# Performance work log

Hardware: AMD Instinct MI355X
Metric: run time of the kernel (lower is better)

## Reference

```python
import jax, jax.numpy as jnp
import numpy as np

N = 8192       # tokens (batch*seq)
D = 4096       # input_size / d_model
H = 256        # gate hidden_size
E = 64         # num_experts
K = 2          # top_k


def setup_inputs() -> dict:
    key = jax.random.key(0)
    k0, k1, k2, k3 = jax.random.split(key, 4)
    x = jax.random.normal(k0, (N, D), dtype=jnp.float32)
    # nn.Linear default init: U(-1/sqrt(fan_in), 1/sqrt(fan_in))
    w1 = jax.random.uniform(k1, (H, D), jnp.float32, -1.0, 1.0) / np.sqrt(D)
    b1 = jax.random.uniform(k2, (H,), jnp.float32, -1.0, 1.0) / np.sqrt(D)
    w2 = jax.random.uniform(k3, (E, H), jnp.float32, -1.0, 1.0) / np.sqrt(H)
    return {"x": x, "w1": w1, "b1": b1, "w2": w2}


def reference(x, w1, b1, w2):
    # MLP gate: Linear -> GELU (exact erf, torch default) -> Dropout(eval: identity) -> Linear(no bias)
    h = jax.nn.gelu(jnp.einsum('nd,hd->nh', x, w1) + b1, approximate=False)  # [N, H]
    logits = jnp.einsum('nh,eh->ne', h, w2)                                  # [N, E]
    probs = jax.nn.softmax(logits, axis=-1)                                  # [N, E]
    # deterministic top-k path (sample_topk=0 / eval mode)
    top_k_gates, top_k_indices = jax.lax.top_k(probs, K)                     # [N, K] each
    return top_k_indices, top_k_gates, probs
```

## Files before the change

kernel.cpp:

```cpp
#include <hip/hip_runtime.h>
#include <hip/hip_bf16.h>
#include <math.h>

#define NTOK 8192
#define DIN  4096
#define HG   256
#define NE   64
#define SPLITK 4
#define KSTEPS 32
#define TR   16

typedef __attribute__((ext_vector_type(8))) short short8;
typedef __attribute__((ext_vector_type(4))) float f32x4;

__device__ __forceinline__ unsigned short f2bf_rne(float f) {
    union { float f; unsigned int u; } v; v.f = f;
    unsigned int r = v.u + 0x7fffu + ((v.u >> 16) & 1u);
    return (unsigned short)(r >> 16);
}
__device__ __forceinline__ float bf2f(unsigned short b) {
    union { unsigned int u; float f; } v; v.u = ((unsigned int)b) << 16;
    return v.f;
}

typedef const __attribute__((address_space(1))) unsigned int* gptr_t;
typedef __attribute__((address_space(3))) unsigned int* lptr_t;
__device__ __forceinline__ void gload_lds16(const void* g, void* l) {
    __builtin_amdgcn_global_load_lds((gptr_t)g, (lptr_t)l, 16, 0, 0);
}

#define WAIT_VMCNT4 { asm volatile("s_waitcnt vmcnt(4)" ::: "memory"); \
                      __builtin_amdgcn_sched_barrier(0); }
#define WAIT_VMCNT0 { asm volatile("s_waitcnt vmcnt(0)" ::: "memory"); \
                      __builtin_amdgcn_sched_barrier(0); }
#define WAIT_LGKM0  { asm volatile("s_waitcnt lgkmcnt(0)" ::: "memory"); \
                      __builtin_amdgcn_sched_barrier(0); }

__global__ __launch_bounds__(512) void convert_w1_kernel(
    const float* __restrict__ w1, unsigned short* __restrict__ w1t)
{
    const int id    = blockIdx.x * 512 + threadIdx.x;
    const int lane  = id & 63;
    const int cg    = id >> 6;
    const int kstep = cg >> 5;
    const int c     = cg & 31;
    const int hl    = c >> 4;
    const int unit  = c & 15;
    const int n     = unit * 16 + (lane & 15);
    const int k     = kstep * 32 + ((lane >> 4) & 3) * 8;

    const float* src = w1 + (size_t)n * DIN + k;
    short8 v;
#pragma unroll
    for (int j = 0; j < 8; ++j) {
        float f = src[j];
        unsigned short hi = f2bf_rne(f);
        v[j] = (hl == 0) ? (short)hi : (short)f2bf_rne(f - bf2f(hi));
    }
    *(short8*)(w1t + (size_t)cg * 512 + lane * 8) = v;
}

__global__ __launch_bounds__(512, 2) void gemm1_mfma_kernel(
    const float* __restrict__ x, const unsigned short* __restrict__ w1t,
    float* __restrict__ P)
{
    __shared__ unsigned short As[2][2][8][512];
    __shared__ unsigned short Bs[3][2][16][512];

    const int bid  = blockIdx.x;
    const int s    = (bid & 7) >> 1;
    const int mblk = ((bid >> 3) << 1) | (bid & 1);
    const int t    = threadIdx.x;
    const int lane = t & 63;
    const int w    = t >> 6;
    const int wm   = w >> 2;
    const int wn   = w & 3;

    const int m_base = mblk * 128;
    const int kstep0 = s * KSTEPS;

    const int a_unit = t >> 6;
    const int a_q    = t & 63;
    const int a_row  = a_unit * 16 + (a_q & 15);
    const int a_koff = (a_q >> 4) * 8;
    const float* asrc = x + (size_t)(m_base + a_row) * DIN
                          + (size_t)kstep0 * 32 + a_koff;
    const int a_ldso = a_q * 8;

    f32x4 acc[4][4];
#pragma unroll
    for (int i = 0; i < 4; ++i)
#pragma unroll
        for (int j = 0; j < 4; ++j) acc[i][j] = (f32x4)0.f;

#define CVT8_STORE(BUF, F0, F1)                                               \
    {   short8 vh_, vl_;                                                      \
        float ff_[8] = { (F0).x, (F0).y, (F0).z, (F0).w,                      \
                         (F1).x, (F1).y, (F1).z, (F1).w };                    \
        _Pragma("unroll")                                                     \
        for (int j_ = 0; j_ < 8; ++j_) {                                      \
            unsigned short h_ = f2bf_rne(ff_[j_]);                            \
            vh_[j_] = (short)h_;                                              \
            vl_[j_] = (short)f2bf_rne(ff_[j_] - bf2f(h_));                    \
        }                                                                     \
        *(short8*)&As[BUF][0][a_unit][a_ldso] = vh_;                          \
        *(short8*)&As[BUF][1][a_unit][a_ldso] = vl_;                          \
    }

#define ISSUE_B(KS, BUF)                                                      \
    _Pragma("unroll")                                                         \
    for (int i_ = 0; i_ < 4; ++i_) {                                          \
        const int c_ = w * 4 + i_;                                            \
        gload_lds16(w1t + ((size_t)(KS) * 32 + c_) * 512 + lane * 8,          \
                    &Bs[BUF][c_ >> 4][c_ & 15][0]);                           \
    }

    {
        float4 a0 = *(const float4*)(asrc);
        float4 a1 = *(const float4*)(asrc + 4);
        ISSUE_B(kstep0, 0)
        CVT8_STORE(0, a0, a1)
        ISSUE_B(kstep0 + 1, 1)
        WAIT_VMCNT4
        WAIT_LGKM0
        __builtin_amdgcn_s_barrier();
    }

    int bcur = 0, bnx1 = 1, bnx2 = 2;
    int acur = 0;

#pragma unroll 1
    for (int tt = 0; tt < KSTEPS; ++tt) {
        const bool has1 = (tt + 1 < KSTEPS);
        const bool has2 = (tt + 2 < KSTEPS);

        float4 nx0, nx1;
        if (has1) {
            const float* ap = asrc + (size_t)(tt + 1) * 32;
            nx0 = *(const float4*)(ap);
            nx1 = *(const float4*)(ap + 4);
        }
        if (has2) { ISSUE_B(kstep0 + tt + 2, bnx2) }

        short8 ahf[4], alf[4], bhf[4], blf[4];
#pragma unroll
        for (int mr = 0; mr < 4; ++mr) {
            ahf[mr] = *(const short8*)&As[acur][0][wm * 4 + mr][lane * 8];
            alf[mr] = *(const short8*)&As[acur][1][wm * 4 + mr][lane * 8];
        }
#pragma unroll
        for (int nr = 0; nr < 4; ++nr) {
            bhf[nr] = *(const short8*)&Bs[bcur][0][wn * 4 + nr][lane * 8];
            blf[nr] = *(const short8*)&Bs[bcur][1][wn * 4 + nr][lane * 8];
        }

        __builtin_amdgcn_s_setprio(1);
#pragma unroll
        for (int mr = 0; mr < 4; ++mr)
#pragma unroll
            for (int nr = 0; nr < 4; ++nr)
                acc[mr][nr] = __builtin_amdgcn_mfma_f32_16x16x32_bf16(
                    ahf[mr], bhf[nr], acc[mr][nr], 0, 0, 0);
#pragma unroll
        for (int mr = 0; mr < 4; ++mr)
#pragma unroll
            for (int nr = 0; nr < 4; ++nr)
                acc[mr][nr] = __builtin_amdgcn_mfma_f32_16x16x32_bf16(
                    ahf[mr], blf[nr], acc[mr][nr], 0, 0, 0);
#pragma unroll
        for (int mr = 0; mr < 4; ++mr)
#pragma unroll
            for (int nr = 0; nr < 4; ++nr)
                acc[mr][nr] = __builtin_amdgcn_mfma_f32_16x16x32_bf16(
                    alf[mr], bhf[nr], acc[mr][nr], 0, 0, 0);
        __builtin_amdgcn_s_setprio(0);

        if (has1) {
            CVT8_STORE(acur ^ 1, nx0, nx1)
            if (has2) { WAIT_VMCNT4 }
            else      { WAIT_VMCNT0 }
            WAIT_LGKM0
            __builtin_amdgcn_s_barrier();
        }

        const int z = bcur; bcur = bnx1; bnx1 = bnx2; bnx2 = z;
        acur ^= 1;
    }
#undef ISSUE_B
#undef CVT8_STORE

    float* pb = P + (size_t)s * ((size_t)NTOK * HG);
#pragma unroll
    for (int mr = 0; mr < 4; ++mr)
#pragma unroll
        for (int nr = 0; nr < 4; ++nr) {
            const int n = wn * 64 + nr * 16 + (lane & 15);
#pragma unroll
            for (int r = 0; r < 4; ++r) {
                const int m = m_base + wm * 64 + mr * 16 + ((lane >> 4) & 3) * 4 + r;
                pb[(size_t)m * HG + n] = acc[mr][nr][r];
            }
        }
}

__global__ __launch_bounds__(512, 4) void reduce_gate_kernel(
    const float* __restrict__ P, const float* __restrict__ b1,
    const float* __restrict__ w2, float* __restrict__ out)
{
    __shared__ float h_lds[TR][260];
    __shared__ float lg[NE][33];

    const int t    = threadIdx.x;
    const int lane = t & 63;
    const int w    = t >> 6;
    const int r0   = blockIdx.x * TR;
    const size_t SS = (size_t)NTOK * HG;

    {
        const int row = t >> 5;
        const int sg  = t & 31;
        const size_t base = (size_t)(r0 + row) * HG + sg * 8;

        float q[8];
#pragma unroll
        for (int half = 0; half < 2; ++half) {
            float4 v0 = *(const float4*)(P + base + half * 4);
            float4 v1 = *(const float4*)(P + base + SS + half * 4);
            float4 v2 = *(const float4*)(P + base + 2 * SS + half * 4);
            float4 v3 = *(const float4*)(P + base + 3 * SS + half * 4);
            float4 bb = *(const float4*)(b1 + sg * 8 + half * 4);
            q[half * 4 + 0] = v0.x + v1.x + v2.x + v3.x + bb.x;
            q[half * 4 + 1] = v0.y + v1.y + v2.y + v3.y + bb.y;
            q[half * 4 + 2] = v0.z + v1.z + v2.z + v3.z + bb.z;
            q[half * 4 + 3] = v0.w + v1.w + v2.w + v3.w + bb.w;
        }
#pragma unroll
        for (int c = 0; c < 8; ++c)
            q[c] = 0.5f * q[c] * (1.0f + erff(q[c] * 0.70710678118654752440f));

        *(float4*)&h_lds[row][sg * 8]     = make_float4(q[0], q[1], q[2], q[3]);
        *(float4*)&h_lds[row][sg * 8 + 4] = make_float4(q[4], q[5], q[6], q[7]);
    }
    __syncthreads();

    const int e0   = w * 8;
    const int rowp = lane & 15;
    const int kq   = lane >> 4;

    float acc[8];
#pragma unroll
    for (int i = 0; i < 8; ++i) acc[i] = 0.f;

    const float* w2b = w2 + (size_t)e0 * HG + kq * 64;
#pragma unroll 1
    for (int kc = 0; kc < 64; kc += 8) {
        float a[8];
        *(float4*)&a[0] = *(const float4*)&h_lds[rowp][kq * 64 + kc];
        *(float4*)&a[4] = *(const float4*)&h_lds[rowp][kq * 64 + kc + 4];
#pragma unroll
        for (int n = 0; n < 8; ++n) {
            const float* wr = w2b + (size_t)n * HG + kc;
            float4 w0 = *(const float4*)(wr);
            float4 w1v = *(const float4*)(wr + 4);
            acc[n] = fmaf(w0.x, a[0], acc[n]);
            acc[n] = fmaf(w0.y, a[1], acc[n]);
            acc[n] = fmaf(w0.z, a[2], acc[n]);
            acc[n] = fmaf(w0.w, a[3], acc[n]);
            acc[n] = fmaf(w1v.x, a[4], acc[n]);
            acc[n] = fmaf(w1v.y, a[5], acc[n]);
            acc[n] = fmaf(w1v.z, a[6], acc[n]);
            acc[n] = fmaf(w1v.w, a[7], acc[n]);
        }
    }
#pragma unroll
    for (int n = 0; n < 8; ++n) {
        acc[n] += __shfl_xor(acc[n], 16);
        acc[n] += __shfl_xor(acc[n], 32);
    }
    if (lane < 16) {
#pragma unroll
        for (int n = 0; n < 8; ++n) lg[e0 + n][rowp] = acc[n];
    }
    __syncthreads();

    if (t < TR) {
        float l[NE];
#pragma unroll
        for (int e = 0; e < NE; ++e) l[e] = lg[e][t];

        float mx = l[0];
#pragma unroll
        for (int e = 1; e < NE; ++e) mx = fmaxf(mx, l[e]);

        float ssum = 0.f;
#pragma unroll
        for (int e = 0; e < NE; ++e) { float p = expf(l[e] - mx); l[e] = p; ssum += p; }
        const float inv = 1.0f / ssum;
#pragma unroll
        for (int e = 0; e < NE; ++e) l[e] *= inv;

        float v1 = -1.0f, v2 = -2.0f;
        int   i1 = 0,     i2 = 0;
#pragma unroll
        for (int e = 0; e < NE; ++e) {
            const float p  = l[e];
            const bool  g1 = p > v1;
            const bool  g2 = p > v2;
            const float nv2 = g1 ? v1 : (g2 ? p : v2);
            const int   ni2 = g1 ? i1 : (g2 ? e : i2);
            v1 = g1 ? p : v1;
            i1 = g1 ? e : i1;
            v2 = nv2;
            i2 = ni2;
        }

        const int row = r0 + t;
        float* out_idx  = out;
        float* out_gate = out + 2 * NTOK;
        float* out_prob = out + 4 * NTOK;
        out_idx[2 * row + 0]  = (float)i1;
        out_idx[2 * row + 1]  = (float)i2;
        out_gate[2 * row + 0] = v1;
        out_gate[2 * row + 1] = v2;

        float* pr = out_prob + (size_t)row * NE;
#pragma unroll
        for (int e = 0; e < NE; e += 4)
            *(float4*)(pr + e) = make_float4(l[e], l[e + 1], l[e + 2], l[e + 3]);
    }
}

extern "C" void kernel_launch(void* const* d_in, const int* in_sizes, int n_in,
                              void* d_out, int out_size, void* d_ws, size_t ws_size,
                              hipStream_t stream) {
    const float* x  = (const float*)d_in[0];
    const float* w1 = (const float*)d_in[1];
    const float* b1 = (const float*)d_in[2];
    const float* w2 = (const float*)d_in[3];
    float* out = (float*)d_out;

    unsigned short* w1t = (unsigned short*)d_ws;
    float* P = (float*)((char*)d_ws + (4u << 20));

    convert_w1_kernel<<<512, 512, 0, stream>>>(w1, w1t);
    gemm1_mfma_kernel<<<256, 512, 0, stream>>>(x, w1t, P);
    reduce_gate_kernel<<<512, 512, 0, stream>>>(P, b1, w2, out);
}
```

Baseline: 104.3 us.

## Shrink GEMM1 tiles to 64 rows and drop multi-buffered async B pipeline

```diff
diff --git a/kernel.cpp b/kernel.cpp
--- a/kernel.cpp
+++ b/kernel.cpp
@@ -29,8 +29,6 @@
     __builtin_amdgcn_global_load_lds((gptr_t)g, (lptr_t)l, 16, 0, 0);
 }
 
-#define WAIT_VMCNT4 { asm volatile("s_waitcnt vmcnt(4)" ::: "memory"); \
-                      __builtin_amdgcn_sched_barrier(0); }
 #define WAIT_VMCNT0 { asm volatile("s_waitcnt vmcnt(0)" ::: "memory"); \
                       __builtin_amdgcn_sched_barrier(0); }
 #define WAIT_LGKM0  { asm volatile("s_waitcnt lgkmcnt(0)" ::: "memory"); \
@@ -60,23 +58,21 @@
     *(short8*)(w1t + (size_t)cg * 512 + lane * 8) = v;
 }
 
-__global__ __launch_bounds__(512, 2) void gemm1_mfma_kernel(
+__global__ __launch_bounds__(256, 4) void gemm1_mfma_kernel(
     const float* __restrict__ x, const unsigned short* __restrict__ w1t,
     float* __restrict__ P)
 {
-    __shared__ unsigned short As[2][2][8][512];
-    __shared__ unsigned short Bs[3][2][16][512];
+    __shared__ unsigned short As[2][4][512];
+    __shared__ unsigned short Bs[2][16][512];
 
     const int bid  = blockIdx.x;
-    const int s    = (bid & 7) >> 1;
-    const int mblk = ((bid >> 3) << 1) | (bid & 1);
+    const int mblk = bid & 127;
+    const int s    = bid >> 7;
     const int t    = threadIdx.x;
     const int lane = t & 63;
     const int w    = t >> 6;
-    const int wm   = w >> 2;
-    const int wn   = w & 3;
-
-    const int m_base = mblk * 128;
+
+    const int m_base = mblk * 64;
     const int kstep0 = s * KSTEPS;
 
     const int a_unit = t >> 6;
@@ -93,7 +89,7 @@
 #pragma unroll
         for (int j = 0; j < 4; ++j) acc[i][j] = (f32x4)0.f;
 
-#define CVT8_STORE(BUF, F0, F1)                                               \
+#define CVT8_STORE(F0, F1)                                                    \
     {   short8 vh_, vl_;                                                      \
         float ff_[8] = { (F0).x, (F0).y, (F0).z, (F0).w,                      \
                          (F1).x, (F1).y, (F1).z, (F1).w };                    \
@@ -103,36 +99,31 @@
             vh_[j_] = (short)h_;                                              \
             vl_[j_] = (short)f2bf_rne(ff_[j_] - bf2f(h_));                    \
         }                                                                     \
-        *(short8*)&As[BUF][0][a_unit][a_ldso] = vh_;                          \
-        *(short8*)&As[BUF][1][a_unit][a_ldso] = vl_;                          \
-    }
-
-#define ISSUE_B(KS, BUF)                                                      \
+        *(short8*)&As[0][a_unit][a_ldso] = vh_;                               \
+        *(short8*)&As[1][a_unit][a_ldso] = vl_;                               \
+    }
+
+#define ISSUE_B(KS)                                                           \
     _Pragma("unroll")                                                         \
-    for (int i_ = 0; i_ < 4; ++i_) {                                          \
-        const int c_ = w * 4 + i_;                                            \
+    for (int i_ = 0; i_ < 8; ++i_) {                                          \
+        const int c_ = w * 8 + i_;                                            \
         gload_lds16(w1t + ((size_t)(KS) * 32 + c_) * 512 + lane * 8,          \
-                    &Bs[BUF][c_ >> 4][c_ & 15][0]);                           \
+                    &Bs[c_ >> 4][c_ & 15][0]);                                \
     }
 
     {
         float4 a0 = *(const float4*)(asrc);
         float4 a1 = *(const float4*)(asrc + 4);
-        ISSUE_B(kstep0, 0)
-        CVT8_STORE(0, a0, a1)
-        ISSUE_B(kstep0 + 1, 1)
-        WAIT_VMCNT4
+        ISSUE_B(kstep0)
+        CVT8_STORE(a0, a1)
+        WAIT_VMCNT0
         WAIT_LGKM0
         __builtin_amdgcn_s_barrier();
     }
-
-    int bcur = 0, bnx1 = 1, bnx2 = 2;
-    int acur = 0;
 
 #pragma unroll 1
     for (int tt = 0; tt < KSTEPS; ++tt) {
         const bool has1 = (tt + 1 < KSTEPS);
-        const bool has2 = (tt + 2 < KSTEPS);
 
         float4 nx0, nx1;
         if (has1) {
@@ -140,18 +131,17 @@
             nx0 = *(const float4*)(ap);
             nx1 = *(const float4*)(ap + 4);
         }
-        if (has2) { ISSUE_B(kstep0 + tt + 2, bnx2) }
 
         short8 ahf[4], alf[4], bhf[4], blf[4];
 #pragma unroll
         for (int mr = 0; mr < 4; ++mr) {
-            ahf[mr] = *(const short8*)&As[acur][0][wm * 4 + mr][lane * 8];
-            alf[mr] = *(const short8*)&As[acur][1][wm * 4 + mr][lane * 8];
+            ahf[mr] = *(const short8*)&As[0][mr][lane * 8];
+            alf[mr] = *(const short8*)&As[1][mr][lane * 8];
         }
 #pragma unroll
         for (int nr = 0; nr < 4; ++nr) {
-            bhf[nr] = *(const short8*)&Bs[bcur][0][wn * 4 + nr][lane * 8];
-            blf[nr] = *(const short8*)&Bs[bcur][1][wn * 4 + nr][lane * 8];
+            bhf[nr] = *(const short8*)&Bs[0][w * 4 + nr][lane * 8];
+            blf[nr] = *(const short8*)&Bs[1][w * 4 + nr][lane * 8];
         }
 
         __builtin_amdgcn_s_setprio(1);
@@ -176,15 +166,16 @@
         __builtin_amdgcn_s_setprio(0);
 
         if (has1) {
-            CVT8_STORE(acur ^ 1, nx0, nx1)
-            if (has2) { WAIT_VMCNT4 }
-            else      { WAIT_VMCNT0 }
             WAIT_LGKM0
             __builtin_amdgcn_s_barrier();
-        }
-
-        const int z = bcur; bcur = bnx1; bnx1 = bnx2; bnx2 = z;
-        acur ^= 1;
+
+            ISSUE_B(kstep0 + tt + 1)
+            CVT8_STORE(nx0, nx1)
+
+            WAIT_VMCNT0
+            WAIT_LGKM0
+            __builtin_amdgcn_s_barrier();
+        }
     }
 #undef ISSUE_B
 #undef CVT8_STORE
@@ -194,10 +185,10 @@
     for (int mr = 0; mr < 4; ++mr)
 #pragma unroll
         for (int nr = 0; nr < 4; ++nr) {
-            const int n = wn * 64 + nr * 16 + (lane & 15);
+            const int n = w * 64 + nr * 16 + (lane & 15);
 #pragma unroll
             for (int r = 0; r < 4; ++r) {
-                const int m = m_base + wm * 64 + mr * 16 + ((lane >> 4) & 3) * 4 + r;
+                const int m = m_base + mr * 16 + ((lane >> 4) & 3) * 4 + r;
                 pb[(size_t)m * HG + n] = acc[mr][nr][r];
             }
         }
@@ -343,6 +334,6 @@
     float* P = (float*)((char*)d_ws + (4u << 20));
 
     convert_w1_kernel<<<512, 512, 0, stream>>>(w1, w1t);
-    gemm1_mfma_kernel<<<256, 512, 0, stream>>>(x, w1t, P);
+    gemm1_mfma_kernel<<<512, 256, 0, stream>>>(x, w1t, P);
     reduce_gate_kernel<<<512, 512, 0, stream>>>(P, b1, w2, out);
 }
```

Result: slower. 186.3 us (+78.7%).

## Restructure GEMM1 main loop into two-phase ping-pong schedule with double-buffered B

Applied to the files above, without the earlier changes.

```diff
diff --git a/kernel.cpp b/kernel.cpp
--- a/kernel.cpp
+++ b/kernel.cpp
@@ -29,7 +29,7 @@
     __builtin_amdgcn_global_load_lds((gptr_t)g, (lptr_t)l, 16, 0, 0);
 }
 
-#define WAIT_VMCNT4 { asm volatile("s_waitcnt vmcnt(4)" ::: "memory"); \
+#define WAIT_VMCNT2 { asm volatile("s_waitcnt vmcnt(2)" ::: "memory"); \
                       __builtin_amdgcn_sched_barrier(0); }
 #define WAIT_VMCNT0 { asm volatile("s_waitcnt vmcnt(0)" ::: "memory"); \
                       __builtin_amdgcn_sched_barrier(0); }
@@ -65,11 +65,11 @@
     float* __restrict__ P)
 {
     __shared__ unsigned short As[2][2][8][512];
-    __shared__ unsigned short Bs[3][2][16][512];
+    __shared__ unsigned short Bs[2][2][16][512];
 
     const int bid  = blockIdx.x;
-    const int s    = (bid & 7) >> 1;
-    const int mblk = ((bid >> 3) << 1) | (bid & 1);
+    const int mblk = bid & 63;
+    const int s    = bid >> 6;
     const int t    = threadIdx.x;
     const int lane = t & 63;
     const int w    = t >> 6;
@@ -115,76 +115,101 @@
                     &Bs[BUF][c_ >> 4][c_ & 15][0]);                           \
     }
 
+    float4 nxc0, nxc1;
     {
+        ISSUE_B(kstep0, 0)
         float4 a0 = *(const float4*)(asrc);
         float4 a1 = *(const float4*)(asrc + 4);
-        ISSUE_B(kstep0, 0)
         CVT8_STORE(0, a0, a1)
-        ISSUE_B(kstep0 + 1, 1)
-        WAIT_VMCNT4
+        nxc0 = *(const float4*)(asrc + 32);
+        nxc1 = *(const float4*)(asrc + 36);
         WAIT_LGKM0
         __builtin_amdgcn_s_barrier();
     }
 
-    int bcur = 0, bnx1 = 1, bnx2 = 2;
-    int acur = 0;
+    int cur = 0;
 
 #pragma unroll 1
     for (int tt = 0; tt < KSTEPS; ++tt) {
         const bool has1 = (tt + 1 < KSTEPS);
         const bool has2 = (tt + 2 < KSTEPS);
 
-        float4 nx0, nx1;
+        short8 bh[4], bl[4], ah0, al0, ah1, al1;
+#pragma unroll
+        for (int nr = 0; nr < 4; ++nr) {
+            bh[nr] = *(const short8*)&Bs[cur][0][wn * 4 + nr][lane * 8];
+            bl[nr] = *(const short8*)&Bs[cur][1][wn * 4 + nr][lane * 8];
+        }
+        ah0 = *(const short8*)&As[cur][0][wm * 4 + 0][lane * 8];
+        al0 = *(const short8*)&As[cur][1][wm * 4 + 0][lane * 8];
+        ah1 = *(const short8*)&As[cur][0][wm * 4 + 1][lane * 8];
+        al1 = *(const short8*)&As[cur][1][wm * 4 + 1][lane * 8];
+
+        if (has1) { ISSUE_B(kstep0 + tt + 1, cur ^ 1) }
+        float4 nxn0, nxn1;
+        if (has2) {
+            const float* ap = asrc + (size_t)(tt + 2) * 32;
+            nxn0 = *(const float4*)(ap);
+            nxn1 = *(const float4*)(ap + 4);
+        }
+
+        __builtin_amdgcn_s_barrier();
+        WAIT_LGKM0
+        __builtin_amdgcn_s_setprio(1);
+#pragma unroll
+        for (int nr = 0; nr < 4; ++nr) {
+            acc[0][nr] = __builtin_amdgcn_mfma_f32_16x16x32_bf16(ah0, bh[nr], acc[0][nr], 0, 0, 0);
+            acc[1][nr] = __builtin_amdgcn_mfma_f32_16x16x32_bf16(ah1, bh[nr], acc[1][nr], 0, 0, 0);
+        }
+#pragma unroll
+        for (int nr = 0; nr < 4; ++nr) {
+            acc[0][nr] = __builtin_amdgcn_mfma_f32_16x16x32_bf16(ah0, bl[nr], acc[0][nr], 0, 0, 0);
+            acc[1][nr] = __builtin_amdgcn_mfma_f32_16x16x32_bf16(ah1, bl[nr], acc[1][nr], 0, 0, 0);
+        }
+#pragma unroll
+        for (int nr = 0; nr < 4; ++nr) {
+            acc[0][nr] = __builtin_amdgcn_mfma_f32_16x16x32_bf16(al0, bh[nr], acc[0][nr], 0, 0, 0);
+            acc[1][nr] = __builtin_amdgcn_mfma_f32_16x16x32_bf16(al1, bh[nr], acc[1][nr], 0, 0, 0);
+        }
+        __builtin_amdgcn_s_setprio(0);
+        __builtin_amdgcn_s_barrier();
+
+        short8 ah2, al2, ah3, al3;
+        ah2 = *(const short8*)&As[cur][0][wm * 4 + 2][lane * 8];
+        al2 = *(const short8*)&As[cur][1][wm * 4 + 2][lane * 8];
+        ah3 = *(const short8*)&As[cur][0][wm * 4 + 3][lane * 8];
+        al3 = *(const short8*)&As[cur][1][wm * 4 + 3][lane * 8];
+
+        if (has1) { CVT8_STORE(cur ^ 1, nxc0, nxc1) }
+
+        __builtin_amdgcn_s_barrier();
+        WAIT_LGKM0
+        __builtin_amdgcn_s_setprio(1);
+#pragma unroll
+        for (int nr = 0; nr < 4; ++nr) {
+            acc[2][nr] = __builtin_amdgcn_mfma_f32_16x16x32_bf16(ah2, bh[nr], acc[2][nr], 0, 0, 0);
+            acc[3][nr] = __builtin_amdgcn_mfma_f32_16x16x32_bf16(ah3, bh[nr], acc[3][nr], 0, 0, 0);
+        }
+#pragma unroll
+        for (int nr = 0; nr < 4; ++nr) {
+            acc[2][nr] = __builtin_amdgcn_mfma_f32_16x16x32_bf16(ah2, bl[nr], acc[2][nr], 0, 0, 0);
+            acc[3][nr] = __builtin_amdgcn_mfma_f32_16x16x32_bf16(ah3, bl[nr], acc[3][nr], 0, 0, 0);
+        }
+#pragma unroll
+        for (int nr = 0; nr < 4; ++nr) {
+            acc[2][nr] = __builtin_amdgcn_mfma_f32_16x16x32_bf16(al2, bh[nr], acc[2][nr], 0, 0, 0);
+            acc[3][nr] = __builtin_amdgcn_mfma_f32_16x16x32_bf16(al3, bh[nr], acc[3][nr], 0, 0, 0);
+        }
+        __builtin_amdgcn_s_setprio(0);
+
         if (has1) {
-            const float* ap = asrc + (size_t)(tt + 1) * 32;
-            nx0 = *(const float4*)(ap);
-            nx1 = *(const float4*)(ap + 4);
-        }
-        if (has2) { ISSUE_B(kstep0 + tt + 2, bnx2) }
-
-        short8 ahf[4], alf[4], bhf[4], blf[4];
-#pragma unroll
-        for (int mr = 0; mr < 4; ++mr) {
-            ahf[mr] = *(const short8*)&As[acur][0][wm * 4 + mr][lane * 8];
-            alf[mr] = *(const short8*)&As[acur][1][wm * 4 + mr][lane * 8];
-        }
-#pragma unroll
-        for (int nr = 0; nr < 4; ++nr) {
-            bhf[nr] = *(const short8*)&Bs[bcur][0][wn * 4 + nr][lane * 8];
-            blf[nr] = *(const short8*)&Bs[bcur][1][wn * 4 + nr][lane * 8];
-        }
-
-        __builtin_amdgcn_s_setprio(1);
-#pragma unroll
-        for (int mr = 0; mr < 4; ++mr)
-#pragma unroll
-            for (int nr = 0; nr < 4; ++nr)
-                acc[mr][nr] = __builtin_amdgcn_mfma_f32_16x16x32_bf16(
-                    ahf[mr], bhf[nr], acc[mr][nr], 0, 0, 0);
-#pragma unroll
-        for (int mr = 0; mr < 4; ++mr)
-#pragma unroll
-            for (int nr = 0; nr < 4; ++nr)
-                acc[mr][nr] = __builtin_amdgcn_mfma_f32_16x16x32_bf16(
-                    ahf[mr], blf[nr], acc[mr][nr], 0, 0, 0);
-#pragma unroll
-        for (int mr = 0; mr < 4; ++mr)
-#pragma unroll
-            for (int nr = 0; nr < 4; ++nr)
-                acc[mr][nr] = __builtin_amdgcn_mfma_f32_16x16x32_bf16(
-                    alf[mr], bhf[nr], acc[mr][nr], 0, 0, 0);
-        __builtin_amdgcn_s_setprio(0);
-
-        if (has1) {
-            CVT8_STORE(acur ^ 1, nx0, nx1)
-            if (has2) { WAIT_VMCNT4 }
+            if (has2) { WAIT_VMCNT2 }
             else      { WAIT_VMCNT0 }
-            WAIT_LGKM0
-            __builtin_amdgcn_s_barrier();
-        }
-
-        const int z = bcur; bcur = bnx1; bnx1 = bnx2; bnx2 = z;
-        acur ^= 1;
+        }
+        __builtin_amdgcn_s_barrier();
+
+        nxc0 = nxn0; nxc1 = nxn1;
+        cur ^= 1;
     }
 #undef ISSUE_B
 #undef CVT8_STORE
```

Result: faster. 92.82 us (-11.0%).

## Restructure GEMM1 main loop into four barrier-separated MFMA phases with double buffering

Applied to the files above, without the earlier changes.

```diff
diff --git a/kernel.cpp b/kernel.cpp
--- a/kernel.cpp
+++ b/kernel.cpp
@@ -29,8 +29,6 @@
     __builtin_amdgcn_global_load_lds((gptr_t)g, (lptr_t)l, 16, 0, 0);
 }
 
-#define WAIT_VMCNT4 { asm volatile("s_waitcnt vmcnt(4)" ::: "memory"); \
-                      __builtin_amdgcn_sched_barrier(0); }
 #define WAIT_VMCNT0 { asm volatile("s_waitcnt vmcnt(0)" ::: "memory"); \
                       __builtin_amdgcn_sched_barrier(0); }
 #define WAIT_LGKM0  { asm volatile("s_waitcnt lgkmcnt(0)" ::: "memory"); \
@@ -65,11 +63,11 @@
     float* __restrict__ P)
 {
     __shared__ unsigned short As[2][2][8][512];
-    __shared__ unsigned short Bs[3][2][16][512];
+    __shared__ unsigned short Bs[2][2][16][512];
 
     const int bid  = blockIdx.x;
-    const int s    = (bid & 7) >> 1;
-    const int mblk = ((bid >> 3) << 1) | (bid & 1);
+    const int s    = bid & 3;
+    const int mblk = bid >> 2;
     const int t    = threadIdx.x;
     const int lane = t & 63;
     const int w    = t >> 6;
@@ -115,77 +113,93 @@
                     &Bs[BUF][c_ >> 4][c_ & 15][0]);                           \
     }
 
+#define MFMA_PHASE(NR, BH, BL)                                                \
+    {   _Pragma("unroll")                                                     \
+        for (int mr_ = 0; mr_ < 4; ++mr_)                                     \
+            acc[mr_][NR] = __builtin_amdgcn_mfma_f32_16x16x32_bf16(           \
+                ah[mr_], BH, acc[mr_][NR], 0, 0, 0);                          \
+        _Pragma("unroll")                                                     \
+        for (int mr_ = 0; mr_ < 4; ++mr_)                                     \
+            acc[mr_][NR] = __builtin_amdgcn_mfma_f32_16x16x32_bf16(           \
+                ah[mr_], BL, acc[mr_][NR], 0, 0, 0);                          \
+        _Pragma("unroll")                                                     \
+        for (int mr_ = 0; mr_ < 4; ++mr_)                                     \
+            acc[mr_][NR] = __builtin_amdgcn_mfma_f32_16x16x32_bf16(           \
+                al[mr_], BH, acc[mr_][NR], 0, 0, 0);                          \
+    }
+
     {
-        float4 a0 = *(const float4*)(asrc);
-        float4 a1 = *(const float4*)(asrc + 4);
         ISSUE_B(kstep0, 0)
-        CVT8_STORE(0, a0, a1)
-        ISSUE_B(kstep0 + 1, 1)
-        WAIT_VMCNT4
-        WAIT_LGKM0
-        __builtin_amdgcn_s_barrier();
-    }
-
-    int bcur = 0, bnx1 = 1, bnx2 = 2;
-    int acur = 0;
+        float4 p0 = *(const float4*)(asrc);
+        float4 p1 = *(const float4*)(asrc + 4);
+        CVT8_STORE(0, p0, p1)
+        WAIT_VMCNT0
+        WAIT_LGKM0
+        __builtin_amdgcn_s_barrier();
+    }
+
+    int cur = 0;
 
 #pragma unroll 1
     for (int tt = 0; tt < KSTEPS; ++tt) {
         const bool has1 = (tt + 1 < KSTEPS);
-        const bool has2 = (tt + 2 < KSTEPS);
-
+        const int  nxt  = cur ^ 1;
+
+        short8 ah[4], al[4];
         float4 nx0, nx1;
+
+#pragma unroll
+        for (int mr = 0; mr < 4; ++mr) {
+            ah[mr] = *(const short8*)&As[cur][0][wm * 4 + mr][lane * 8];
+            al[mr] = *(const short8*)&As[cur][1][wm * 4 + mr][lane * 8];
+        }
+        short8 bh = *(const short8*)&Bs[cur][0][wn * 4 + 0][lane * 8];
+        short8 bl = *(const short8*)&Bs[cur][1][wn * 4 + 0][lane * 8];
         if (has1) {
             const float* ap = asrc + (size_t)(tt + 1) * 32;
             nx0 = *(const float4*)(ap);
             nx1 = *(const float4*)(ap + 4);
-        }
-        if (has2) { ISSUE_B(kstep0 + tt + 2, bnx2) }
-
-        short8 ahf[4], alf[4], bhf[4], blf[4];
-#pragma unroll
-        for (int mr = 0; mr < 4; ++mr) {
-            ahf[mr] = *(const short8*)&As[acur][0][wm * 4 + mr][lane * 8];
-            alf[mr] = *(const short8*)&As[acur][1][wm * 4 + mr][lane * 8];
-        }
-#pragma unroll
-        for (int nr = 0; nr < 4; ++nr) {
-            bhf[nr] = *(const short8*)&Bs[bcur][0][wn * 4 + nr][lane * 8];
-            blf[nr] = *(const short8*)&Bs[bcur][1][wn * 4 + nr][lane * 8];
-        }
-
+            ISSUE_B(kstep0 + tt + 1, nxt)
+        }
+        __builtin_amdgcn_s_barrier();
+        WAIT_LGKM0
         __builtin_amdgcn_s_setprio(1);
-#pragma unroll
-        for (int mr = 0; mr < 4; ++mr)
-#pragma unroll
-            for (int nr = 0; nr < 4; ++nr)
-                acc[mr][nr] = __builtin_amdgcn_mfma_f32_16x16x32_bf16(
-                    ahf[mr], bhf[nr], acc[mr][nr], 0, 0, 0);
-#pragma unroll
-        for (int mr = 0; mr < 4; ++mr)
-#pragma unroll
-            for (int nr = 0; nr < 4; ++nr)
-                acc[mr][nr] = __builtin_amdgcn_mfma_f32_16x16x32_bf16(
-                    ahf[mr], blf[nr], acc[mr][nr], 0, 0, 0);
-#pragma unroll
-        for (int mr = 0; mr < 4; ++mr)
-#pragma unroll
-            for (int nr = 0; nr < 4; ++nr)
-                acc[mr][nr] = __builtin_amdgcn_mfma_f32_16x16x32_bf16(
-                    alf[mr], bhf[nr], acc[mr][nr], 0, 0, 0);
+        MFMA_PHASE(0, bh, bl)
         __builtin_amdgcn_s_setprio(0);
-
-        if (has1) {
-            CVT8_STORE(acur ^ 1, nx0, nx1)
-            if (has2) { WAIT_VMCNT4 }
-            else      { WAIT_VMCNT0 }
-            WAIT_LGKM0
-            __builtin_amdgcn_s_barrier();
-        }
-
-        const int z = bcur; bcur = bnx1; bnx1 = bnx2; bnx2 = z;
-        acur ^= 1;
-    }
+        __builtin_amdgcn_s_barrier();
+
+        bh = *(const short8*)&Bs[cur][0][wn * 4 + 1][lane * 8];
+        bl = *(const short8*)&Bs[cur][1][wn * 4 + 1][lane * 8];
+        __builtin_amdgcn_s_barrier();
+        WAIT_LGKM0
+        __builtin_amdgcn_s_setprio(1);
+        MFMA_PHASE(1, bh, bl)
+        __builtin_amdgcn_s_setprio(0);
+        __builtin_amdgcn_s_barrier();
+
+        bh = *(const short8*)&Bs[cur][0][wn * 4 + 2][lane * 8];
+        bl = *(const short8*)&Bs[cur][1][wn * 4 + 2][lane * 8];
+        if (has1) { CVT8_STORE(nxt, nx0, nx1) }
+        __builtin_amdgcn_s_barrier();
+        WAIT_LGKM0
+        __builtin_amdgcn_s_setprio(1);
+        MFMA_PHASE(2, bh, bl)
+        __builtin_amdgcn_s_setprio(0);
+        __builtin_amdgcn_s_barrier();
+
+        bh = *(const short8*)&Bs[cur][0][wn * 4 + 3][lane * 8];
+        bl = *(const short8*)&Bs[cur][1][wn * 4 + 3][lane * 8];
+        __builtin_amdgcn_s_barrier();
+        WAIT_LGKM0
+        __builtin_amdgcn_s_setprio(1);
+        MFMA_PHASE(3, bh, bl)
+        __builtin_amdgcn_s_setprio(0);
+        WAIT_VMCNT0
+        __builtin_amdgcn_s_barrier();
+
+        cur ^= 1;
+    }
+#undef MFMA_PHASE
 #undef ISSUE_B
 #undef CVT8_STORE
 
```

Result: no change. 105.2 us (+0.9%).
